# Optimization experiments

Measured on AMD Instinct MI355X. Metric: run time of the kernel, lower is better.

The kernel has to match this reference:

```python
import jax, jax.numpy as jnp
import numpy as np

EPS = 1e-5
GROUPS = 32


def setup_inputs() -> dict:
    key = jax.random.key(0)
    ks = jax.random.split(key, 12)
    b, c, h, w = 8, 256, 64, 64
    s = 1.0 / np.sqrt(c)
    return {
        "x": jax.random.normal(ks[0], (b, c, h, w), jnp.float32),
        "gn_w": jax.random.uniform(ks[1], (c,), jnp.float32, 0.5, 1.5),
        "gn_b": jax.random.normal(ks[2], (c,), jnp.float32) * 0.1,
        "wq": jax.random.normal(ks[3], (c, c), jnp.float32) * s,
        "bq": jax.random.normal(ks[4], (c,), jnp.float32) * 0.02,
        "wk": jax.random.normal(ks[5], (c, c), jnp.float32) * s,
        "bk": jax.random.normal(ks[6], (c,), jnp.float32) * 0.02,
        "wv": jax.random.normal(ks[7], (c, c), jnp.float32) * s,
        "bv": jax.random.normal(ks[8], (c,), jnp.float32) * 0.02,
        "wp": jax.random.normal(ks[9], (c, c), jnp.float32) * s,
        "bp": jax.random.normal(ks[10], (c,), jnp.float32) * 0.02,
        "gamma": jax.random.normal(ks[11], (1,), jnp.float32),
    }


def _group_norm(x, weight, bias):
    b, c, h, w = x.shape
    g = min(c, GROUPS)
    xg = x.reshape(b, g, c // g, h * w)
    mean = xg.mean(axis=(2, 3), keepdims=True)
    var = jnp.var(xg, axis=(2, 3), keepdims=True)
    xn = (xg - mean) * jax.lax.rsqrt(var + EPS)
    xn = xn.reshape(b, c, h, w)
    return xn * weight[None, :, None, None] + bias[None, :, None, None]


def reference(x, gn_w, gn_b, wq, bq, wk, bk, wv, bv, wp, bp, gamma):
    b, c, h, w = x.shape
    x_dash = _group_norm(x, gn_w, gn_b)           # (b,c,h,w)
    xf = x_dash.reshape(b, c, h * w)              # (b,c,n)
    # 1x1 convs == per-pixel linear maps over channels
    q = jnp.einsum('oc,bcn->bon', wq, xf) + bq[None, :, None]
    k = jnp.einsum('oc,bcn->bon', wk, xf) + bk[None, :, None]
    v = jnp.einsum('oc,bcn->bon', wv, xf) + bv[None, :, None]
    # attn[b,i,j] = <q[:,i], k[:,j]> / sqrt(c)
    attn = jnp.einsum('bci,bcj->bij', q, k) / jnp.sqrt(jnp.asarray(c, x.dtype))
    attn = jax.nn.softmax(attn, axis=-1)
    # out[b,c,i] = sum_j v[b,c,j] * attn[b,i,j]
    out = jnp.einsum('bcj,bij->bci', v, attn)
    out = jnp.einsum('oc,bcn->bon', wp, out) + bp[None, :, None]
    out = out.reshape(b, c, h, w)
    return x + gamma[0] * out
```

## Files before the change

kernel.cpp:

```cpp
#include <hip/hip_runtime.h>
#include <cstdint>
#include <cstddef>


#define NB   8
#define NC   256
#define NPIX 4096
#define CPG  8

typedef __attribute__((ext_vector_type(8))) short bf16x8;
typedef __attribute__((ext_vector_type(4))) short s16x4;
typedef __attribute__((ext_vector_type(8))) short s16x8;
typedef __attribute__((ext_vector_type(4))) float f32x4;

__device__ __forceinline__ short f2bf(float f) {
  union { float f; uint32_t u; } v; v.f = f;
  return (short)((v.u + 0x7fffu + ((v.u >> 16) & 1u)) >> 16);
}

__device__ __forceinline__ uint32_t cvtpk_bf(float a, float b) {
  uint32_t r;
  asm("v_cvt_pk_bf16_f32 %0, %1, %2" : "=v"(r) : "v"(a), "v"(b));
  return r;
}

__device__ __forceinline__ f32x4 mfma16(bf16x8 a, bf16x8 b, f32x4 c) {
  return __builtin_amdgcn_mfma_f32_16x16x32_bf16(a, b, c, 0, 0, 0);
}

__device__ __forceinline__ void gload_lds16(const short* g, short* l) {
  __builtin_amdgcn_global_load_lds(
      (const __attribute__((address_space(1))) void*)g,
      (__attribute__((address_space(3))) void*)l, 16, 0, 0);
}

__global__ __launch_bounds__(256) void wconv4(
    const float* __restrict__ w0, const float* __restrict__ w1,
    const float* __restrict__ w2, const float* __restrict__ w3,
    short* __restrict__ o0, short* __restrict__ o1,
    short* __restrict__ o2, short* __restrict__ o3) {
  int m = blockIdx.x >> 6;
  const float* w = (m == 0) ? w0 : (m == 1) ? w1 : (m == 2) ? w2 : w3;
  short* o = (m == 0) ? o0 : (m == 1) ? o1 : (m == 2) ? o2 : o3;
  int i = ((blockIdx.x & 63) * 256 + threadIdx.x) * 4;
  float4 v = *reinterpret_cast<const float4*>(w + i);
  s16x4 p;
  p[0] = f2bf(v.x); p[1] = f2bf(v.y); p[2] = f2bf(v.z); p[3] = f2bf(v.w);
  *reinterpret_cast<s16x4*>(o + i) = p;
}

__global__ __launch_bounds__(256) void gnorm(const float* __restrict__ x,
                                             const float* __restrict__ gw,
                                             const float* __restrict__ gb,
                                             short* __restrict__ xdt) {
  int b = blockIdx.x >> 5;
  int g = blockIdx.x & 31;
  const float* xp = x + ((size_t)b * NC + (size_t)g * CPG) * NPIX;
  int t = threadIdx.x;

  float s = 0.f, ss = 0.f;
  const float4* xp4 = reinterpret_cast<const float4*>(xp);
  for (int i = t; i < (CPG * NPIX) / 4; i += 256) {
    float4 v = xp4[i];
    s  += v.x + v.y + v.z + v.w;
    ss += v.x * v.x + v.y * v.y + v.z * v.z + v.w * v.w;
  }
  for (int m = 32; m; m >>= 1) { s += __shfl_xor(s, m); ss += __shfl_xor(ss, m); }
  __shared__ float red[10];
  int wid = t >> 6;
  if ((t & 63) == 0) { red[wid] = s; red[4 + wid] = ss; }
  __syncthreads();
  if (t == 0) {
    float a  = red[0] + red[1] + red[2] + red[3];
    float b2 = red[4] + red[5] + red[6] + red[7];
    float mean = a * (1.f / 32768.f);
    float var  = b2 * (1.f / 32768.f) - mean * mean;
    red[8] = mean;
    red[9] = rsqrtf(var + 1e-5f);
  }
  __syncthreads();
  float mean = red[8], rstd = red[9];

  float wv2[CPG], bv2[CPG];
  for (int cc = 0; cc < CPG; ++cc) {
    float wgt = gw[g * CPG + cc] * rstd;
    wv2[cc] = wgt;
    bv2[cc] = gb[g * CPG + cc] - mean * wgt;
  }
  for (int pix = t; pix < NPIX; pix += 256) {
    s16x8 pk;
    for (int cc = 0; cc < CPG; ++cc)
      pk[cc] = f2bf(fmaf(xp[cc * NPIX + pix], wv2[cc], bv2[cc]));
    *reinterpret_cast<s16x8*>(&xdt[((size_t)b * NPIX + pix) * NC + g * CPG]) = pk;
  }
}

__global__ __launch_bounds__(256) void qkv_gemm(
    const short* __restrict__ wq_bf, const short* __restrict__ wk_bf,
    const short* __restrict__ wv_bf,
    const float* __restrict__ bq, const float* __restrict__ bk,
    const float* __restrict__ bv,
    const short* __restrict__ xdt,
    short* __restrict__ qt, short* __restrict__ kt, short* __restrict__ vv) {
  int nt = blockIdx.x, b = blockIdx.y;

  __shared__ short xtile[64 * 256];
  __shared__ float bias_lds[3][256];
  int t = threadIdx.x;
  const short* xg = xdt + ((size_t)b * NPIX + nt * 64) * NC;
  for (int it = 0; it < 8; ++it) {
    int id = t + it * 256, row = id >> 5, part = id & 31;
    *reinterpret_cast<uint4*>(&xtile[row * 256 + (part ^ (row & 7)) * 8]) =
        *reinterpret_cast<const uint4*>(&xg[(size_t)row * 256 + part * 8]);
  }
  bias_lds[0][t] = bq[t];
  bias_lds[1][t] = bk[t];
  bias_lds[2][t] = bv[t];
  __syncthreads();

  int w = t >> 6, lane = t & 63, g = lane >> 4, lr = lane & 15;
  const short* Ws[3] = {wq_bf, wk_bf, wv_bf};

  for (int mi = 0; mi < 3; ++mi) {
    const short* W = Ws[mi];
    f32x4 acc[4][4];
    f32x4 zz = {0.f, 0.f, 0.f, 0.f};
    for (int i = 0; i < 4; ++i) for (int j = 0; j < 4; ++j) acc[i][j] = zz;

    for (int c0 = 0; c0 < 256; c0 += 32) {
      bf16x8 af[4], bfr[4];
      for (int mf = 0; mf < 4; ++mf)
        af[mf] = *reinterpret_cast<const bf16x8*>(
            &W[(size_t)(w * 64 + mf * 16 + lr) * 256 + c0 + g * 8]);
      for (int nf = 0; nf < 4; ++nf) {
        int row = nf * 16 + lr;
        bfr[nf] = *reinterpret_cast<const bf16x8*>(
            &xtile[row * 256 + (((c0 >> 3) + g) ^ (row & 7)) * 8]);
      }
      for (int mf = 0; mf < 4; ++mf)
        for (int nf = 0; nf < 4; ++nf)
          acc[mf][nf] = mfma16(af[mf], bfr[nf], acc[mf][nf]);
    }

    if (mi < 2) {
      short* outp = (mi == 0) ? qt : kt;
      for (int mf = 0; mf < 4; ++mf)
        for (int nf = 0; nf < 4; ++nf) {
          int ob = w * 64 + mf * 16 + g * 4;
          int n  = nt * 64 + nf * 16 + lr;
          s16x4 pk;
          for (int r = 0; r < 4; ++r)
            pk[r] = f2bf(acc[mf][nf][r] + bias_lds[mi][ob + r]);
          *reinterpret_cast<s16x4*>(&outp[((size_t)b * NPIX + n) * NC + ob]) = pk;
        }
    } else {
      for (int mf = 0; mf < 4; ++mf)
        for (int nf = 0; nf < 4; ++nf) {
          int ob = w * 64 + mf * 16 + g * 4;
          int n  = nt * 64 + nf * 16 + lr;
          for (int r = 0; r < 4; ++r)
            vv[((size_t)b * NC + ob + r) * NPIX + n] =
                f2bf(acc[mf][nf][r] + bias_lds[2][ob + r]);
        }
    }
  }
}

__global__ __launch_bounds__(256, 2) void attn(
    const short* __restrict__ qt, const short* __restrict__ kt,
    const short* __restrict__ vv, short* __restrict__ ot) {
  int b = blockIdx.x, itile = blockIdx.y;
  __shared__ short ktile[64 * 256];
  __shared__ short Pb[2][64 * 64];
  __shared__ float alpha_lds[2][64];
  __shared__ float exch[2][64];

  int t = threadIdx.x, w = t >> 6, lane = t & 63, g = lane >> 4, lr = lane & 15;
  int kk = w >> 1, qq = w & 1;
  int i0 = itile * 64;

  const short* ktg = kt + (size_t)b * NPIX * NC;

  for (int it = 0; it < 8; ++it) {
    int id = it * 256 + t, row = id >> 5, ch = id & 31;
    gload_lds16(ktg + row * 256 + (ch ^ (row & 7)) * 8, &ktile[id * 8]);
  }
  const short* kgp = ktg + 16384;

  bf16x8 qf[2][8];
  for (int qi = 0; qi < 2; ++qi) {
    const short* qrow =
        qt + ((size_t)b * NPIX + i0 + 32 * qq + 16 * qi + lr) * NC;
    for (int ks = 0; ks < 8; ++ks)
      qf[qi][ks] = *reinterpret_cast<const bf16x8*>(&qrow[ks * 32 + g * 8]);
  }

  const short* vp = vv + (size_t)b * NC * NPIX + (size_t)(w * 64 + lr) * NPIX + g * 8;

  int row0 = 32 * kk + lr, row1 = row0 + 16;
  int eidx[2], pwo[2][2];
  for (int qi = 0; qi < 2; ++qi) {
    int q_loc = 32 * qq + 16 * qi + lr;
    eidx[qi] = q_loc;
    for (int mt = 0; mt < 2; ++mt)
      pwo[qi][mt] = q_loc * 64 +
                    (((4 * kk + 2 * mt + (g >> 1)) ^ (q_loc & 7)) * 8) +
                    (g & 1) * 4;
  }
  int pr[4][2];
  for (int nf = 0; nf < 4; ++nf)
    for (int ks2 = 0; ks2 < 2; ++ks2) {
      int qc = nf * 16 + lr;
      pr[nf][ks2] = qc * 64 + (((ks2 * 4 + g) ^ (qc & 7)) * 8);
    }

  f32x4 zz = {0.f, 0.f, 0.f, 0.f};
  f32x4 oacc[4][4];
  for (int i = 0; i < 4; ++i) for (int j = 0; j < 4; ++j) oacc[i][j] = zz;
  bf16x8 va[2][4];
  float m_[2] = {-1e30f, -1e30f}, l_p[2] = {0.f, 0.f};

  const float sc = 0.0625f, L2E = 1.44269504f;
  const float SCL = sc * L2E;

  for (int jt = 0; jt < 64; ++jt) {
    int cur = jt & 1, prv = cur ^ 1;

    asm volatile("s_waitcnt vmcnt(0) lgkmcnt(0)" ::: "memory");
    __builtin_amdgcn_s_barrier();
    asm volatile("" ::: "memory");

    if (jt > 0) {
      float av[4];
      for (int nf = 0; nf < 4; ++nf) av[nf] = alpha_lds[prv][nf * 16 + lr];
      if (__any((av[0] != 1.f) | (av[1] != 1.f) | (av[2] != 1.f) | (av[3] != 1.f))) {
        for (int mf = 0; mf < 4; ++mf)
          for (int nf = 0; nf < 4; ++nf) oacc[mf][nf] *= av[nf];
      }
      __builtin_amdgcn_s_setprio(1);
      for (int ks2 = 0; ks2 < 2; ++ks2) {
        bf16x8 pb[4];
        for (int nf = 0; nf < 4; ++nf)
          pb[nf] = *reinterpret_cast<const bf16x8*>(&Pb[prv][pr[nf][ks2]]);
        for (int mf = 0; mf < 4; ++mf)
          for (int nf = 0; nf < 4; ++nf)
            oacc[mf][nf] = mfma16(va[ks2][mf], pb[nf], oacc[mf][nf]);
      }
      __builtin_amdgcn_s_setprio(0);
    }

    for (int ks2 = 0; ks2 < 2; ++ks2)
      for (int mf = 0; mf < 4; ++mf)
        va[ks2][mf] = *reinterpret_cast<const bf16x8*>(
            vp + (size_t)mf * (16 * NPIX) + ks2 * 32);
    vp += 64;

    f32x4 s[2][2];
    s[0][0] = zz; s[0][1] = zz; s[1][0] = zz; s[1][1] = zz;
    __builtin_amdgcn_s_setprio(1);
    for (int ks = 0; ks < 8; ++ks) {
      bf16x8 kf0 = *reinterpret_cast<const bf16x8*>(
          &ktile[row0 * 256 + (((ks * 4) + g) ^ (row0 & 7)) * 8]);
      bf16x8 kf1 = *reinterpret_cast<const bf16x8*>(
          &ktile[row1 * 256 + (((ks * 4) + g) ^ (row1 & 7)) * 8]);
      s[0][0] = mfma16(kf0, qf[0][ks], s[0][0]);
      s[0][1] = mfma16(kf0, qf[1][ks], s[0][1]);
      s[1][0] = mfma16(kf1, qf[0][ks], s[1][0]);
      s[1][1] = mfma16(kf1, qf[1][ks], s[1][1]);
    }
    __builtin_amdgcn_s_setprio(0);

    float mx[2];
    for (int qi = 0; qi < 2; ++qi) {
      float m0 = fmaxf(fmaxf(s[0][qi][0], s[0][qi][1]),
                       fmaxf(s[0][qi][2], s[0][qi][3]));
      float m1 = fmaxf(fmaxf(s[1][qi][0], s[1][qi][1]),
                       fmaxf(s[1][qi][2], s[1][qi][3]));
      float m = fmaxf(m0, m1);
      m = fmaxf(m, __shfl_xor(m, 16));
      m = fmaxf(m, __shfl_xor(m, 32));
      mx[qi] = m;
    }
    if (lane < 16) {
      exch[kk][32 * qq + lr]      = mx[0];
      exch[kk][32 * qq + 16 + lr] = mx[1];
    }

    asm volatile("s_waitcnt lgkmcnt(0)" ::: "memory");
    __builtin_amdgcn_s_barrier();
    asm volatile("" ::: "memory");

    for (int it = 0; it < 8; ++it) {
      int id = it * 256 + t, row = id >> 5, ch = id & 31;
      gload_lds16(kgp + row * 256 + (ch ^ (row & 7)) * 8, &ktile[id * 8]);
    }
    kgp += 16384;

    for (int qi = 0; qi < 2; ++qi) {
      float pm = fmaxf(mx[qi], exch[kk ^ 1][eidx[qi]]) * sc;
      float mn = (pm - m_[qi] <= 8.f) ? m_[qi] : pm;
      float alpha = exp2f((m_[qi] - mn) * L2E);
      float mnl = mn * L2E;
      float ps = 0.f;
      for (int mt = 0; mt < 2; ++mt) {
        float p0 = exp2f(fmaf(s[mt][qi][0], SCL, -mnl));
        float p1 = exp2f(fmaf(s[mt][qi][1], SCL, -mnl));
        float p2 = exp2f(fmaf(s[mt][qi][2], SCL, -mnl));
        float p3 = exp2f(fmaf(s[mt][qi][3], SCL, -mnl));
        ps += p0 + p1 + p2 + p3;
        uint2 pk;
        pk.x = cvtpk_bf(p0, p1);
        pk.y = cvtpk_bf(p2, p3);
        *reinterpret_cast<uint2*>(&Pb[cur][pwo[qi][mt]]) = pk;
      }
      l_p[qi] = l_p[qi] * alpha + ps;
      m_[qi] = mn;
      if (kk == 0 && lane < 16) alpha_lds[cur][eidx[qi]] = alpha;
    }
  }

  asm volatile("s_waitcnt vmcnt(0) lgkmcnt(0)" ::: "memory");
  __builtin_amdgcn_s_barrier();
  asm volatile("" ::: "memory");
  {
    float av[4];
    for (int nf = 0; nf < 4; ++nf) av[nf] = alpha_lds[1][nf * 16 + lr];
    if (__any((av[0] != 1.f) | (av[1] != 1.f) | (av[2] != 1.f) | (av[3] != 1.f))) {
      for (int mf = 0; mf < 4; ++mf)
        for (int nf = 0; nf < 4; ++nf) oacc[mf][nf] *= av[nf];
    }
    for (int ks2 = 0; ks2 < 2; ++ks2) {
      bf16x8 pb[4];
      for (int nf = 0; nf < 4; ++nf)
        pb[nf] = *reinterpret_cast<const bf16x8*>(&Pb[1][pr[nf][ks2]]);
      for (int mf = 0; mf < 4; ++mf)
        for (int nf = 0; nf < 4; ++nf)
          oacc[mf][nf] = mfma16(va[ks2][mf], pb[nf], oacc[mf][nf]);
    }
  }

  for (int qi = 0; qi < 2; ++qi) {
    float v = l_p[qi];
    v += __shfl_xor(v, 16);
    v += __shfl_xor(v, 32);
    l_p[qi] = v;
  }
  if (lane < 16) {
    exch[kk][32 * qq + lr]      = l_p[0];
    exch[kk][32 * qq + 16 + lr] = l_p[1];
  }
  __syncthreads();

  for (int nf = 0; nf < 4; ++nf) {
    int q = nf * 16 + lr;
    float inv = 1.f / (exch[0][q] + exch[1][q]);
    int i = i0 + q;
    for (int mf = 0; mf < 4; ++mf) {
      int cb = w * 64 + mf * 16 + g * 4;
      s16x4 pk;
      for (int r = 0; r < 4; ++r) pk[r] = f2bf(oacc[mf][nf][r] * inv);
      *reinterpret_cast<s16x4*>(&ot[((size_t)b * NPIX + i) * NC + cb]) = pk;
    }
  }
}

__global__ __launch_bounds__(256) void proj_res(
    const short* __restrict__ wp_bf, const float* __restrict__ bp,
    const short* __restrict__ ot, const float* __restrict__ x,
    const float* __restrict__ gamma, float* __restrict__ out) {
  int nt = blockIdx.x, b = blockIdx.y;
  __shared__ short otile[64 * 256];
  __shared__ float bias_lds[256];
  int t = threadIdx.x;
  const short* og = ot + ((size_t)b * NPIX + nt * 64) * NC;
  for (int itx = 0; itx < 8; ++itx) {
    int id = t + itx * 256, row = id >> 5, part = id & 31;
    *reinterpret_cast<uint4*>(&otile[row * 256 + (part ^ (row & 7)) * 8]) =
        *reinterpret_cast<const uint4*>(&og[(size_t)row * 256 + part * 8]);
  }
  bias_lds[t] = bp[t];
  __syncthreads();

  int w = t >> 6, lane = t & 63, g = lane >> 4, lr = lane & 15;
  f32x4 acc[4][4];
  f32x4 zz = {0.f, 0.f, 0.f, 0.f};
  for (int i = 0; i < 4; ++i) for (int j = 0; j < 4; ++j) acc[i][j] = zz;

  for (int c0 = 0; c0 < 256; c0 += 32) {
    bf16x8 af[4], bfr[4];
    for (int mf = 0; mf < 4; ++mf)
      af[mf] = *reinterpret_cast<const bf16x8*>(
          &wp_bf[(size_t)(w * 64 + mf * 16 + lr) * 256 + c0 + g * 8]);
    for (int nf = 0; nf < 4; ++nf) {
      int row = nf * 16 + lr;
      bfr[nf] = *reinterpret_cast<const bf16x8*>(
          &otile[row * 256 + (((c0 >> 3) + g) ^ (row & 7)) * 8]);
    }
    for (int mf = 0; mf < 4; ++mf)
      for (int nf = 0; nf < 4; ++nf)
        acc[mf][nf] = mfma16(af[mf], bfr[nf], acc[mf][nf]);
  }

  float gm = gamma[0];
  for (int mf = 0; mf < 4; ++mf)
    for (int nf = 0; nf < 4; ++nf) {
      int ob = w * 64 + mf * 16 + g * 4;
      int n  = nt * 64 + nf * 16 + lr;
      for (int r = 0; r < 4; ++r) {
        size_t idx = ((size_t)b * NC + ob + r) * NPIX + n;
        out[idx] = x[idx] + gm * (acc[mf][nf][r] + bias_lds[ob + r]);
      }
    }
}

extern "C" void kernel_launch(void* const* d_in, const int* in_sizes, int n_in,
                              void* d_out, int out_size, void* d_ws, size_t ws_size,
                              hipStream_t stream) {
  (void)in_sizes; (void)n_in; (void)out_size; (void)ws_size;
  const float* x     = (const float*)d_in[0];
  const float* gn_w  = (const float*)d_in[1];
  const float* gn_b  = (const float*)d_in[2];
  const float* wq    = (const float*)d_in[3];
  const float* bq    = (const float*)d_in[4];
  const float* wk    = (const float*)d_in[5];
  const float* bk    = (const float*)d_in[6];
  const float* wv    = (const float*)d_in[7];
  const float* bv    = (const float*)d_in[8];
  const float* wp    = (const float*)d_in[9];
  const float* bp    = (const float*)d_in[10];
  const float* gamma = (const float*)d_in[11];
  float* out = (float*)d_out;

  char* ws = (char*)d_ws;
  const size_t WSZ = 131072;
  const size_t TSZ = (size_t)NB * NPIX * NC * 2;
  short* wq_bf = (short*)(ws);
  short* wk_bf = (short*)(ws + WSZ);
  short* wv_bf = (short*)(ws + 2 * WSZ);
  short* wp_bf = (short*)(ws + 3 * WSZ);
  short* xdt   = (short*)(ws + 4 * WSZ);
  short* qt    = (short*)(ws + 4 * WSZ + TSZ);
  short* kt    = (short*)(ws + 4 * WSZ + 2 * TSZ);
  short* vv    = (short*)(ws + 4 * WSZ + 3 * TSZ);
  short* ot    = xdt;

  wconv4<<<256, 256, 0, stream>>>(wq, wk, wv, wp, wq_bf, wk_bf, wv_bf, wp_bf);

  gnorm<<<256, 256, 0, stream>>>(x, gn_w, gn_b, xdt);

  qkv_gemm<<<dim3(64, 8), 256, 0, stream>>>(wq_bf, wk_bf, wv_bf, bq, bk, bv,
                                            xdt, qt, kt, vv);

  attn<<<dim3(8, 64), 256, 0, stream>>>(qt, kt, vv, ot);

  proj_res<<<dim3(64, 8), 256, 0, stream>>>(wp_bf, bp, ot, x, gamma, out);
}
```

Baseline: 316.8 us.

## Decouple per-half-key softmax state in attention and widen groupnorm blocks

The attention kernel now keeps separate running max, sum and output accumulators for each pair of waves covering a key half. This removes the per-tile cross-wave max exchange through shared memory, and the max update and rescale run only when a score exceeds a lazy threshold. The PV MFMAs are split so each half's accumulation sits on a different side of the barrier, and the two partial results are merged with exp-weighted combination at the end. This doubles the output accumulator registers, which risks register pressure and spills at two blocks per CU. Separately, groupnorm runs with 1024-thread blocks instead of 256.

```diff
diff --git a/kernel.cpp b/kernel.cpp
--- a/kernel.cpp
+++ b/kernel.cpp
@@ -49,10 +49,10 @@
   *reinterpret_cast<s16x4*>(o + i) = p;
 }
 
-__global__ __launch_bounds__(256) void gnorm(const float* __restrict__ x,
-                                             const float* __restrict__ gw,
-                                             const float* __restrict__ gb,
-                                             short* __restrict__ xdt) {
+__global__ __launch_bounds__(1024) void gnorm(const float* __restrict__ x,
+                                              const float* __restrict__ gw,
+                                              const float* __restrict__ gb,
+                                              short* __restrict__ xdt) {
   int b = blockIdx.x >> 5;
   int g = blockIdx.x & 31;
   const float* xp = x + ((size_t)b * NC + (size_t)g * CPG) * NPIX;
@@ -60,26 +60,26 @@
 
   float s = 0.f, ss = 0.f;
   const float4* xp4 = reinterpret_cast<const float4*>(xp);
-  for (int i = t; i < (CPG * NPIX) / 4; i += 256) {
+  for (int i = t; i < (CPG * NPIX) / 4; i += 1024) {
     float4 v = xp4[i];
     s  += v.x + v.y + v.z + v.w;
     ss += v.x * v.x + v.y * v.y + v.z * v.z + v.w * v.w;
   }
   for (int m = 32; m; m >>= 1) { s += __shfl_xor(s, m); ss += __shfl_xor(ss, m); }
-  __shared__ float red[10];
+  __shared__ float red[34];
   int wid = t >> 6;
-  if ((t & 63) == 0) { red[wid] = s; red[4 + wid] = ss; }
+  if ((t & 63) == 0) { red[wid] = s; red[16 + wid] = ss; }
   __syncthreads();
   if (t == 0) {
-    float a  = red[0] + red[1] + red[2] + red[3];
-    float b2 = red[4] + red[5] + red[6] + red[7];
+    float a = 0.f, b2 = 0.f;
+    for (int i = 0; i < 16; ++i) { a += red[i]; b2 += red[16 + i]; }
     float mean = a * (1.f / 32768.f);
     float var  = b2 * (1.f / 32768.f) - mean * mean;
-    red[8] = mean;
-    red[9] = rsqrtf(var + 1e-5f);
+    red[32] = mean;
+    red[33] = rsqrtf(var + 1e-5f);
   }
   __syncthreads();
-  float mean = red[8], rstd = red[9];
+  float mean = red[32], rstd = red[33];
 
   float wv2[CPG], bv2[CPG];
   for (int cc = 0; cc < CPG; ++cc) {
@@ -87,7 +87,7 @@
     wv2[cc] = wgt;
     bv2[cc] = gb[g * CPG + cc] - mean * wgt;
   }
-  for (int pix = t; pix < NPIX; pix += 256) {
+  for (int pix = t; pix < NPIX; pix += 1024) {
     s16x8 pk;
     for (int cc = 0; cc < CPG; ++cc)
       pk[cc] = f2bf(fmaf(xp[cc * NPIX + pix], wv2[cc], bv2[cc]));
@@ -172,8 +172,9 @@
   int b = blockIdx.x, itile = blockIdx.y;
   __shared__ short ktile[64 * 256];
   __shared__ short Pb[2][64 * 64];
-  __shared__ float alpha_lds[2][64];
-  __shared__ float exch[2][64];
+  __shared__ float alpha_lds[2][2][64];
+  __shared__ float mfin[2][64];
+  __shared__ float lfin[2][64];
 
   int t = threadIdx.x, w = t >> 6, lane = t & 63, g = lane >> 4, lr = lane & 15;
   int kk = w >> 1, qq = w & 1;
@@ -195,17 +196,17 @@
       qf[qi][ks] = *reinterpret_cast<const bf16x8*>(&qrow[ks * 32 + g * 8]);
   }
 
-  const short* vp = vv + (size_t)b * NC * NPIX + (size_t)(w * 64 + lr) * NPIX + g * 8;
+  const short* vbase =
+      vv + (size_t)b * NC * NPIX + (size_t)(w * 64 + lr) * NPIX + g * 8;
 
   int row0 = 32 * kk + lr, row1 = row0 + 16;
-  int eidx[2], pwo[2][2];
-  for (int qi = 0; qi < 2; ++qi) {
-    int q_loc = 32 * qq + 16 * qi + lr;
-    eidx[qi] = q_loc;
-    for (int mt = 0; mt < 2; ++mt)
-      pwo[qi][mt] = q_loc * 64 +
-                    (((4 * kk + 2 * mt + (g >> 1)) ^ (q_loc & 7)) * 8) +
-                    (g & 1) * 4;
+  int pwo00, pwo01, pwo10, pwo11;
+  {
+    int q0 = 32 * qq + lr, q1 = q0 + 16;
+    pwo00 = q0 * 64 + (((4 * kk + 0 + (g >> 1)) ^ (q0 & 7)) * 8) + (g & 1) * 4;
+    pwo01 = q0 * 64 + (((4 * kk + 2 + (g >> 1)) ^ (q0 & 7)) * 8) + (g & 1) * 4;
+    pwo10 = q1 * 64 + (((4 * kk + 0 + (g >> 1)) ^ (q1 & 7)) * 8) + (g & 1) * 4;
+    pwo11 = q1 * 64 + (((4 * kk + 2 + (g >> 1)) ^ (q1 & 7)) * 8) + (g & 1) * 4;
   }
   int pr[4][2];
   for (int nf = 0; nf < 4; ++nf)
@@ -215,10 +216,13 @@
     }
 
   f32x4 zz = {0.f, 0.f, 0.f, 0.f};
-  f32x4 oacc[4][4];
-  for (int i = 0; i < 4; ++i) for (int j = 0; j < 4; ++j) oacc[i][j] = zz;
-  bf16x8 va[2][4];
-  float m_[2] = {-1e30f, -1e30f}, l_p[2] = {0.f, 0.f};
+  f32x4 oacc0[4][4], oacc1[4][4];
+  for (int i = 0; i < 4; ++i)
+    for (int j = 0; j < 4; ++j) { oacc0[i][j] = zz; oacc1[i][j] = zz; }
+  bf16x8 va0[4], va1[4];
+
+  float m0_ = 0.f, m1_ = 0.f, l0_ = 0.f, l1_ = 0.f;
+  float thr0 = 128.f, thr1 = 128.f;
 
   const float sc = 0.0625f, L2E = 1.44269504f;
   const float SCL = sc * L2E;
@@ -232,59 +236,45 @@
 
     if (jt > 0) {
       float av[4];
-      for (int nf = 0; nf < 4; ++nf) av[nf] = alpha_lds[prv][nf * 16 + lr];
+#pragma unroll
+      for (int nf = 0; nf < 4; ++nf) av[nf] = alpha_lds[prv][0][nf * 16 + lr];
       if (__any((av[0] != 1.f) | (av[1] != 1.f) | (av[2] != 1.f) | (av[3] != 1.f))) {
+#pragma unroll
         for (int mf = 0; mf < 4; ++mf)
-          for (int nf = 0; nf < 4; ++nf) oacc[mf][nf] *= av[nf];
+#pragma unroll
+          for (int nf = 0; nf < 4; ++nf) oacc0[mf][nf] *= av[nf];
       }
       __builtin_amdgcn_s_setprio(1);
-      for (int ks2 = 0; ks2 < 2; ++ks2) {
-        bf16x8 pb[4];
+      bf16x8 pb[4];
+#pragma unroll
+      for (int nf = 0; nf < 4; ++nf)
+        pb[nf] = *reinterpret_cast<const bf16x8*>(&Pb[prv][pr[nf][0]]);
+#pragma unroll
+      for (int mf = 0; mf < 4; ++mf)
+#pragma unroll
         for (int nf = 0; nf < 4; ++nf)
-          pb[nf] = *reinterpret_cast<const bf16x8*>(&Pb[prv][pr[nf][ks2]]);
-        for (int mf = 0; mf < 4; ++mf)
-          for (int nf = 0; nf < 4; ++nf)
-            oacc[mf][nf] = mfma16(va[ks2][mf], pb[nf], oacc[mf][nf]);
-      }
+          oacc0[mf][nf] = mfma16(va0[mf], pb[nf], oacc0[mf][nf]);
       __builtin_amdgcn_s_setprio(0);
-    }
-
-    for (int ks2 = 0; ks2 < 2; ++ks2)
-      for (int mf = 0; mf < 4; ++mf)
-        va[ks2][mf] = *reinterpret_cast<const bf16x8*>(
-            vp + (size_t)mf * (16 * NPIX) + ks2 * 32);
-    vp += 64;
-
-    f32x4 s[2][2];
-    s[0][0] = zz; s[0][1] = zz; s[1][0] = zz; s[1][1] = zz;
+      const short* vp = vbase + (size_t)(jt - 1) * 64 + 32;
+#pragma unroll
+      for (int mf = 0; mf < 4; ++mf)
+        va1[mf] = *reinterpret_cast<const bf16x8*>(vp + (size_t)mf * (16 * NPIX));
+    }
+
+    f32x4 s00 = zz, s01 = zz, s10 = zz, s11 = zz;
     __builtin_amdgcn_s_setprio(1);
+#pragma unroll
     for (int ks = 0; ks < 8; ++ks) {
       bf16x8 kf0 = *reinterpret_cast<const bf16x8*>(
           &ktile[row0 * 256 + (((ks * 4) + g) ^ (row0 & 7)) * 8]);
       bf16x8 kf1 = *reinterpret_cast<const bf16x8*>(
           &ktile[row1 * 256 + (((ks * 4) + g) ^ (row1 & 7)) * 8]);
-      s[0][0] = mfma16(kf0, qf[0][ks], s[0][0]);
-      s[0][1] = mfma16(kf0, qf[1][ks], s[0][1]);
-      s[1][0] = mfma16(kf1, qf[0][ks], s[1][0]);
-      s[1][1] = mfma16(kf1, qf[1][ks], s[1][1]);
+      s00 = mfma16(kf0, qf[0][ks], s00);
+      s01 = mfma16(kf0, qf[1][ks], s01);
+      s10 = mfma16(kf1, qf[0][ks], s10);
+      s11 = mfma16(kf1, qf[1][ks], s11);
     }
     __builtin_amdgcn_s_setprio(0);
-
-    float mx[2];
-    for (int qi = 0; qi < 2; ++qi) {
-      float m0 = fmaxf(fmaxf(s[0][qi][0], s[0][qi][1]),
-                       fmaxf(s[0][qi][2], s[0][qi][3]));
-      float m1 = fmaxf(fmaxf(s[1][qi][0], s[1][qi][1]),
-                       fmaxf(s[1][qi][2], s[1][qi][3]));
-      float m = fmaxf(m0, m1);
-      m = fmaxf(m, __shfl_xor(m, 16));
-      m = fmaxf(m, __shfl_xor(m, 32));
-      mx[qi] = m;
-    }
-    if (lane < 16) {
-      exch[kk][32 * qq + lr]      = mx[0];
-      exch[kk][32 * qq + 16 + lr] = mx[1];
-    }
 
     asm volatile("s_waitcnt lgkmcnt(0)" ::: "memory");
     __builtin_amdgcn_s_barrier();
@@ -296,69 +286,159 @@
     }
     kgp += 16384;
 
-    for (int qi = 0; qi < 2; ++qi) {
-      float pm = fmaxf(mx[qi], exch[kk ^ 1][eidx[qi]]) * sc;
-      float mn = (pm - m_[qi] <= 8.f) ? m_[qi] : pm;
-      float alpha = exp2f((m_[qi] - mn) * L2E);
-      float mnl = mn * L2E;
-      float ps = 0.f;
-      for (int mt = 0; mt < 2; ++mt) {
-        float p0 = exp2f(fmaf(s[mt][qi][0], SCL, -mnl));
-        float p1 = exp2f(fmaf(s[mt][qi][1], SCL, -mnl));
-        float p2 = exp2f(fmaf(s[mt][qi][2], SCL, -mnl));
-        float p3 = exp2f(fmaf(s[mt][qi][3], SCL, -mnl));
-        ps += p0 + p1 + p2 + p3;
-        uint2 pk;
-        pk.x = cvtpk_bf(p0, p1);
-        pk.y = cvtpk_bf(p2, p3);
-        *reinterpret_cast<uint2*>(&Pb[cur][pwo[qi][mt]]) = pk;
+    if (jt > 0) {
+      float av[4];
+#pragma unroll
+      for (int nf = 0; nf < 4; ++nf) av[nf] = alpha_lds[prv][1][nf * 16 + lr];
+      if (__any((av[0] != 1.f) | (av[1] != 1.f) | (av[2] != 1.f) | (av[3] != 1.f))) {
+#pragma unroll
+        for (int mf = 0; mf < 4; ++mf)
+#pragma unroll
+          for (int nf = 0; nf < 4; ++nf) oacc1[mf][nf] *= av[nf];
       }
-      l_p[qi] = l_p[qi] * alpha + ps;
-      m_[qi] = mn;
-      if (kk == 0 && lane < 16) alpha_lds[cur][eidx[qi]] = alpha;
-    }
-  }
-
+      __builtin_amdgcn_s_setprio(1);
+      bf16x8 pb[4];
+#pragma unroll
+      for (int nf = 0; nf < 4; ++nf)
+        pb[nf] = *reinterpret_cast<const bf16x8*>(&Pb[prv][pr[nf][1]]);
+#pragma unroll
+      for (int mf = 0; mf < 4; ++mf)
+#pragma unroll
+        for (int nf = 0; nf < 4; ++nf)
+          oacc1[mf][nf] = mfma16(va1[mf], pb[nf], oacc1[mf][nf]);
+      __builtin_amdgcn_s_setprio(0);
+    }
+
+    {
+      const short* vp = vbase + (size_t)jt * 64;
+#pragma unroll
+      for (int mf = 0; mf < 4; ++mf)
+        va0[mf] = *reinterpret_cast<const bf16x8*>(vp + (size_t)mf * (16 * NPIX));
+    }
+
+    float ym0 = fmaxf(fmaxf(fmaxf(s00[0], s00[1]), fmaxf(s00[2], s00[3])),
+                      fmaxf(fmaxf(s10[0], s10[1]), fmaxf(s10[2], s10[3])));
+    float ym1 = fmaxf(fmaxf(fmaxf(s01[0], s01[1]), fmaxf(s01[2], s01[3])),
+                      fmaxf(fmaxf(s11[0], s11[1]), fmaxf(s11[2], s11[3])));
+    float alpha0 = 1.f, alpha1 = 1.f;
+    if (__any((ym0 > thr0) | (ym1 > thr1))) {
+      float sm0 = fmaxf(ym0, __shfl_xor(ym0, 16));
+      sm0 = fmaxf(sm0, __shfl_xor(sm0, 32));
+      float sm1 = fmaxf(ym1, __shfl_xor(ym1, 16));
+      sm1 = fmaxf(sm1, __shfl_xor(sm1, 32));
+      float mn0 = fmaxf(m0_, sm0 * sc);
+      float mn1 = fmaxf(m1_, sm1 * sc);
+      alpha0 = exp2f((m0_ - mn0) * L2E);
+      alpha1 = exp2f((m1_ - mn1) * L2E);
+      m0_ = mn0; m1_ = mn1;
+      thr0 = (mn0 + 8.f) * 16.f;
+      thr1 = (mn1 + 8.f) * 16.f;
+    }
+    float ml0 = m0_ * L2E, ml1 = m1_ * L2E;
+    float ps0, ps1;
+    {
+      float p0 = exp2f(fmaf(s00[0], SCL, -ml0));
+      float p1 = exp2f(fmaf(s00[1], SCL, -ml0));
+      float p2 = exp2f(fmaf(s00[2], SCL, -ml0));
+      float p3 = exp2f(fmaf(s00[3], SCL, -ml0));
+      ps0 = (p0 + p1) + (p2 + p3);
+      uint2 pk; pk.x = cvtpk_bf(p0, p1); pk.y = cvtpk_bf(p2, p3);
+      *reinterpret_cast<uint2*>(&Pb[cur][pwo00]) = pk;
+      p0 = exp2f(fmaf(s10[0], SCL, -ml0));
+      p1 = exp2f(fmaf(s10[1], SCL, -ml0));
+      p2 = exp2f(fmaf(s10[2], SCL, -ml0));
+      p3 = exp2f(fmaf(s10[3], SCL, -ml0));
+      ps0 += (p0 + p1) + (p2 + p3);
+      pk.x = cvtpk_bf(p0, p1); pk.y = cvtpk_bf(p2, p3);
+      *reinterpret_cast<uint2*>(&Pb[cur][pwo01]) = pk;
+    }
+    {
+      float p0 = exp2f(fmaf(s01[0], SCL, -ml1));
+      float p1 = exp2f(fmaf(s01[1], SCL, -ml1));
+      float p2 = exp2f(fmaf(s01[2], SCL, -ml1));
+      float p3 = exp2f(fmaf(s01[3], SCL, -ml1));
+      ps1 = (p0 + p1) + (p2 + p3);
+      uint2 pk; pk.x = cvtpk_bf(p0, p1); pk.y = cvtpk_bf(p2, p3);
+      *reinterpret_cast<uint2*>(&Pb[cur][pwo10]) = pk;
+      p0 = exp2f(fmaf(s11[0], SCL, -ml1));
+      p1 = exp2f(fmaf(s11[1], SCL, -ml1));
+      p2 = exp2f(fmaf(s11[2], SCL, -ml1));
+      p3 = exp2f(fmaf(s11[3], SCL, -ml1));
+      ps1 += (p0 + p1) + (p2 + p3);
+      pk.x = cvtpk_bf(p0, p1); pk.y = cvtpk_bf(p2, p3);
+      *reinterpret_cast<uint2*>(&Pb[cur][pwo11]) = pk;
+    }
+    l0_ = l0_ * alpha0 + ps0;
+    l1_ = l1_ * alpha1 + ps1;
+    if (lane < 16) {
+      alpha_lds[cur][kk][32 * qq + lane]      = alpha0;
+      alpha_lds[cur][kk][32 * qq + 16 + lane] = alpha1;
+    }
+  }
+
+  {
+    const short* vp = vbase + (size_t)63 * 64 + 32;
+#pragma unroll
+    for (int mf = 0; mf < 4; ++mf)
+      va1[mf] = *reinterpret_cast<const bf16x8*>(vp + (size_t)mf * (16 * NPIX));
+  }
   asm volatile("s_waitcnt vmcnt(0) lgkmcnt(0)" ::: "memory");
   __builtin_amdgcn_s_barrier();
   asm volatile("" ::: "memory");
   {
     float av[4];
-    for (int nf = 0; nf < 4; ++nf) av[nf] = alpha_lds[1][nf * 16 + lr];
+#pragma unroll
+    for (int nf = 0; nf < 4; ++nf) av[nf] = alpha_lds[1][0][nf * 16 + lr];
     if (__any((av[0] != 1.f) | (av[1] != 1.f) | (av[2] != 1.f) | (av[3] != 1.f))) {
       for (int mf = 0; mf < 4; ++mf)
-        for (int nf = 0; nf < 4; ++nf) oacc[mf][nf] *= av[nf];
-    }
-    for (int ks2 = 0; ks2 < 2; ++ks2) {
-      bf16x8 pb[4];
+        for (int nf = 0; nf < 4; ++nf) oacc0[mf][nf] *= av[nf];
+    }
+    bf16x8 pb[4];
+#pragma unroll
+    for (int nf = 0; nf < 4; ++nf)
+      pb[nf] = *reinterpret_cast<const bf16x8*>(&Pb[1][pr[nf][0]]);
+    for (int mf = 0; mf < 4; ++mf)
       for (int nf = 0; nf < 4; ++nf)
-        pb[nf] = *reinterpret_cast<const bf16x8*>(&Pb[1][pr[nf][ks2]]);
-      for (int mf = 0; mf < 4; ++mf)
-        for (int nf = 0; nf < 4; ++nf)
-          oacc[mf][nf] = mfma16(va[ks2][mf], pb[nf], oacc[mf][nf]);
-    }
-  }
-
-  for (int qi = 0; qi < 2; ++qi) {
-    float v = l_p[qi];
-    v += __shfl_xor(v, 16);
-    v += __shfl_xor(v, 32);
-    l_p[qi] = v;
-  }
+        oacc0[mf][nf] = mfma16(va0[mf], pb[nf], oacc0[mf][nf]);
+#pragma unroll
+    for (int nf = 0; nf < 4; ++nf) av[nf] = alpha_lds[1][1][nf * 16 + lr];
+    if (__any((av[0] != 1.f) | (av[1] != 1.f) | (av[2] != 1.f) | (av[3] != 1.f))) {
+      for (int mf = 0; mf < 4; ++mf)
+        for (int nf = 0; nf < 4; ++nf) oacc1[mf][nf] *= av[nf];
+    }
+#pragma unroll
+    for (int nf = 0; nf < 4; ++nf)
+      pb[nf] = *reinterpret_cast<const bf16x8*>(&Pb[1][pr[nf][1]]);
+    for (int mf = 0; mf < 4; ++mf)
+      for (int nf = 0; nf < 4; ++nf)
+        oacc1[mf][nf] = mfma16(va1[mf], pb[nf], oacc1[mf][nf]);
+  }
+
+  l0_ += __shfl_xor(l0_, 16); l0_ += __shfl_xor(l0_, 32);
+  l1_ += __shfl_xor(l1_, 16); l1_ += __shfl_xor(l1_, 32);
   if (lane < 16) {
-    exch[kk][32 * qq + lr]      = l_p[0];
-    exch[kk][32 * qq + 16 + lr] = l_p[1];
+    mfin[kk][32 * qq + lane]      = m0_;
+    mfin[kk][32 * qq + 16 + lane] = m1_;
+    lfin[kk][32 * qq + lane]      = l0_;
+    lfin[kk][32 * qq + 16 + lane] = l1_;
   }
   __syncthreads();
 
   for (int nf = 0; nf < 4; ++nf) {
     int q = nf * 16 + lr;
-    float inv = 1.f / (exch[0][q] + exch[1][q]);
+    float m0 = mfin[0][q], m1 = mfin[1][q];
+    float l0 = lfin[0][q], l1 = lfin[1][q];
+    float M = fmaxf(m0, m1);
+    float f0 = exp2f((m0 - M) * L2E);
+    float f1 = exp2f((m1 - M) * L2E);
+    float inv = 1.f / (f0 * l0 + f1 * l1);
+    f0 *= inv; f1 *= inv;
     int i = i0 + q;
     for (int mf = 0; mf < 4; ++mf) {
       int cb = w * 64 + mf * 16 + g * 4;
       s16x4 pk;
-      for (int r = 0; r < 4; ++r) pk[r] = f2bf(oacc[mf][nf][r] * inv);
+      for (int r = 0; r < 4; ++r)
+        pk[r] = f2bf(f0 * oacc0[mf][nf][r] + f1 * oacc1[mf][nf][r]);
       *reinterpret_cast<s16x4*>(&ot[((size_t)b * NPIX + i) * NC + cb]) = pk;
     }
   }
@@ -446,7 +526,7 @@
 
   wconv4<<<256, 256, 0, stream>>>(wq, wk, wv, wp, wq_bf, wk_bf, wv_bf, wp_bf);
 
-  gnorm<<<256, 256, 0, stream>>>(x, gn_w, gn_b, xdt);
+  gnorm<<<256, 1024, 0, stream>>>(x, gn_w, gn_b, xdt);
 
   qkv_gemm<<<dim3(64, 8), 256, 0, stream>>>(wq_bf, wk_bf, wv_bf, bq, bk, bv,
                                             xdt, qt, kt, vv);
```

Result: slower. 1.007 ms (+218.0%).

## Split PV MFMA across attention loop halves and widen groupnorm blocks

Applied to the files above, without the earlier changes.

The attention loop now splits the P·V MFMA work into two halves. The first half runs before the QK^T scores, and the second runs after the K-tile prefetch is issued, behind a partial vmcnt wait. V fragment loads are staggered into va0/va1 so their global latency overlaps other work. The groupnorm kernel moves from 256 to 1024 threads per block with a wider reduction, to raise memory-level parallelism. Risks include extra register pressure, and a partial vmcnt count that depends on the exact number of outstanding loads.

```diff
diff --git a/kernel.cpp b/kernel.cpp
--- a/kernel.cpp
+++ b/kernel.cpp
@@ -49,10 +49,10 @@
   *reinterpret_cast<s16x4*>(o + i) = p;
 }
 
-__global__ __launch_bounds__(256) void gnorm(const float* __restrict__ x,
-                                             const float* __restrict__ gw,
-                                             const float* __restrict__ gb,
-                                             short* __restrict__ xdt) {
+__global__ __launch_bounds__(1024) void gnorm(const float* __restrict__ x,
+                                              const float* __restrict__ gw,
+                                              const float* __restrict__ gb,
+                                              short* __restrict__ xdt) {
   int b = blockIdx.x >> 5;
   int g = blockIdx.x & 31;
   const float* xp = x + ((size_t)b * NC + (size_t)g * CPG) * NPIX;
@@ -60,26 +60,26 @@
 
   float s = 0.f, ss = 0.f;
   const float4* xp4 = reinterpret_cast<const float4*>(xp);
-  for (int i = t; i < (CPG * NPIX) / 4; i += 256) {
+  for (int i = t; i < (CPG * NPIX) / 4; i += 1024) {
     float4 v = xp4[i];
     s  += v.x + v.y + v.z + v.w;
     ss += v.x * v.x + v.y * v.y + v.z * v.z + v.w * v.w;
   }
   for (int m = 32; m; m >>= 1) { s += __shfl_xor(s, m); ss += __shfl_xor(ss, m); }
-  __shared__ float red[10];
+  __shared__ float red[34];
   int wid = t >> 6;
-  if ((t & 63) == 0) { red[wid] = s; red[4 + wid] = ss; }
+  if ((t & 63) == 0) { red[wid] = s; red[16 + wid] = ss; }
   __syncthreads();
   if (t == 0) {
-    float a  = red[0] + red[1] + red[2] + red[3];
-    float b2 = red[4] + red[5] + red[6] + red[7];
+    float a = 0.f, b2 = 0.f;
+    for (int i = 0; i < 16; ++i) { a += red[i]; b2 += red[16 + i]; }
     float mean = a * (1.f / 32768.f);
     float var  = b2 * (1.f / 32768.f) - mean * mean;
-    red[8] = mean;
-    red[9] = rsqrtf(var + 1e-5f);
+    red[32] = mean;
+    red[33] = rsqrtf(var + 1e-5f);
   }
   __syncthreads();
-  float mean = red[8], rstd = red[9];
+  float mean = red[32], rstd = red[33];
 
   float wv2[CPG], bv2[CPG];
   for (int cc = 0; cc < CPG; ++cc) {
@@ -87,7 +87,7 @@
     wv2[cc] = wgt;
     bv2[cc] = gb[g * CPG + cc] - mean * wgt;
   }
-  for (int pix = t; pix < NPIX; pix += 256) {
+  for (int pix = t; pix < NPIX; pix += 1024) {
     s16x8 pk;
     for (int cc = 0; cc < CPG; ++cc)
       pk[cc] = f2bf(fmaf(xp[cc * NPIX + pix], wv2[cc], bv2[cc]));
@@ -195,7 +195,8 @@
       qf[qi][ks] = *reinterpret_cast<const bf16x8*>(&qrow[ks * 32 + g * 8]);
   }
 
-  const short* vp = vv + (size_t)b * NC * NPIX + (size_t)(w * 64 + lr) * NPIX + g * 8;
+  const short* vbase =
+      vv + (size_t)b * NC * NPIX + (size_t)(w * 64 + lr) * NPIX + g * 8;
 
   int row0 = 32 * kk + lr, row1 = row0 + 16;
   int eidx[2], pwo[2][2];
@@ -217,7 +218,7 @@
   f32x4 zz = {0.f, 0.f, 0.f, 0.f};
   f32x4 oacc[4][4];
   for (int i = 0; i < 4; ++i) for (int j = 0; j < 4; ++j) oacc[i][j] = zz;
-  bf16x8 va[2][4];
+  bf16x8 va0[4], va1[4];
   float m_[2] = {-1e30f, -1e30f}, l_p[2] = {0.f, 0.f};
 
   const float sc = 0.0625f, L2E = 1.44269504f;
@@ -232,32 +233,35 @@
 
     if (jt > 0) {
       float av[4];
+#pragma unroll
       for (int nf = 0; nf < 4; ++nf) av[nf] = alpha_lds[prv][nf * 16 + lr];
       if (__any((av[0] != 1.f) | (av[1] != 1.f) | (av[2] != 1.f) | (av[3] != 1.f))) {
+#pragma unroll
         for (int mf = 0; mf < 4; ++mf)
+#pragma unroll
           for (int nf = 0; nf < 4; ++nf) oacc[mf][nf] *= av[nf];
       }
       __builtin_amdgcn_s_setprio(1);
-      for (int ks2 = 0; ks2 < 2; ++ks2) {
-        bf16x8 pb[4];
+      bf16x8 pb[4];
+#pragma unroll
+      for (int nf = 0; nf < 4; ++nf)
+        pb[nf] = *reinterpret_cast<const bf16x8*>(&Pb[prv][pr[nf][0]]);
+#pragma unroll
+      for (int mf = 0; mf < 4; ++mf)
+#pragma unroll
         for (int nf = 0; nf < 4; ++nf)
-          pb[nf] = *reinterpret_cast<const bf16x8*>(&Pb[prv][pr[nf][ks2]]);
-        for (int mf = 0; mf < 4; ++mf)
-          for (int nf = 0; nf < 4; ++nf)
-            oacc[mf][nf] = mfma16(va[ks2][mf], pb[nf], oacc[mf][nf]);
-      }
+          oacc[mf][nf] = mfma16(va0[mf], pb[nf], oacc[mf][nf]);
       __builtin_amdgcn_s_setprio(0);
-    }
-
-    for (int ks2 = 0; ks2 < 2; ++ks2)
-      for (int mf = 0; mf < 4; ++mf)
-        va[ks2][mf] = *reinterpret_cast<const bf16x8*>(
-            vp + (size_t)mf * (16 * NPIX) + ks2 * 32);
-    vp += 64;
+      const short* vp = vbase + (size_t)(jt - 1) * 64 + 32;
+#pragma unroll
+      for (int mf = 0; mf < 4; ++mf)
+        va1[mf] = *reinterpret_cast<const bf16x8*>(vp + (size_t)mf * (16 * NPIX));
+    }
 
     f32x4 s[2][2];
     s[0][0] = zz; s[0][1] = zz; s[1][0] = zz; s[1][1] = zz;
     __builtin_amdgcn_s_setprio(1);
+#pragma unroll
     for (int ks = 0; ks < 8; ++ks) {
       bf16x8 kf0 = *reinterpret_cast<const bf16x8*>(
           &ktile[row0 * 256 + (((ks * 4) + g) ^ (row0 & 7)) * 8]);
@@ -271,6 +275,7 @@
     __builtin_amdgcn_s_setprio(0);
 
     float mx[2];
+#pragma unroll
     for (int qi = 0; qi < 2; ++qi) {
       float m0 = fmaxf(fmaxf(s[0][qi][0], s[0][qi][1]),
                        fmaxf(s[0][qi][2], s[0][qi][3]));
@@ -296,18 +301,42 @@
     }
     kgp += 16384;
 
+    if (jt > 0) {
+      asm volatile("s_waitcnt vmcnt(8)" ::: "memory");
+      __builtin_amdgcn_s_setprio(1);
+      bf16x8 pb[4];
+#pragma unroll
+      for (int nf = 0; nf < 4; ++nf)
+        pb[nf] = *reinterpret_cast<const bf16x8*>(&Pb[prv][pr[nf][1]]);
+#pragma unroll
+      for (int mf = 0; mf < 4; ++mf)
+#pragma unroll
+        for (int nf = 0; nf < 4; ++nf)
+          oacc[mf][nf] = mfma16(va1[mf], pb[nf], oacc[mf][nf]);
+      __builtin_amdgcn_s_setprio(0);
+    }
+
+    {
+      const short* vp = vbase + (size_t)jt * 64;
+#pragma unroll
+      for (int mf = 0; mf < 4; ++mf)
+        va0[mf] = *reinterpret_cast<const bf16x8*>(vp + (size_t)mf * (16 * NPIX));
+    }
+
+#pragma unroll
     for (int qi = 0; qi < 2; ++qi) {
       float pm = fmaxf(mx[qi], exch[kk ^ 1][eidx[qi]]) * sc;
       float mn = (pm - m_[qi] <= 8.f) ? m_[qi] : pm;
       float alpha = exp2f((m_[qi] - mn) * L2E);
       float mnl = mn * L2E;
       float ps = 0.f;
+#pragma unroll
       for (int mt = 0; mt < 2; ++mt) {
         float p0 = exp2f(fmaf(s[mt][qi][0], SCL, -mnl));
         float p1 = exp2f(fmaf(s[mt][qi][1], SCL, -mnl));
         float p2 = exp2f(fmaf(s[mt][qi][2], SCL, -mnl));
         float p3 = exp2f(fmaf(s[mt][qi][3], SCL, -mnl));
-        ps += p0 + p1 + p2 + p3;
+        ps += (p0 + p1) + (p2 + p3);
         uint2 pk;
         pk.x = cvtpk_bf(p0, p1);
         pk.y = cvtpk_bf(p2, p3);
@@ -319,26 +348,39 @@
     }
   }
 
+  {
+    const short* vp = vbase + (size_t)63 * 64 + 32;
+#pragma unroll
+    for (int mf = 0; mf < 4; ++mf)
+      va1[mf] = *reinterpret_cast<const bf16x8*>(vp + (size_t)mf * (16 * NPIX));
+  }
   asm volatile("s_waitcnt vmcnt(0) lgkmcnt(0)" ::: "memory");
   __builtin_amdgcn_s_barrier();
   asm volatile("" ::: "memory");
   {
     float av[4];
+#pragma unroll
     for (int nf = 0; nf < 4; ++nf) av[nf] = alpha_lds[1][nf * 16 + lr];
     if (__any((av[0] != 1.f) | (av[1] != 1.f) | (av[2] != 1.f) | (av[3] != 1.f))) {
       for (int mf = 0; mf < 4; ++mf)
         for (int nf = 0; nf < 4; ++nf) oacc[mf][nf] *= av[nf];
     }
-    for (int ks2 = 0; ks2 < 2; ++ks2) {
-      bf16x8 pb[4];
+    bf16x8 pb[4];
+#pragma unroll
+    for (int nf = 0; nf < 4; ++nf)
+      pb[nf] = *reinterpret_cast<const bf16x8*>(&Pb[1][pr[nf][0]]);
+    for (int mf = 0; mf < 4; ++mf)
       for (int nf = 0; nf < 4; ++nf)
-        pb[nf] = *reinterpret_cast<const bf16x8*>(&Pb[1][pr[nf][ks2]]);
-      for (int mf = 0; mf < 4; ++mf)
-        for (int nf = 0; nf < 4; ++nf)
-          oacc[mf][nf] = mfma16(va[ks2][mf], pb[nf], oacc[mf][nf]);
-    }
-  }
-
+        oacc[mf][nf] = mfma16(va0[mf], pb[nf], oacc[mf][nf]);
+#pragma unroll
+    for (int nf = 0; nf < 4; ++nf)
+      pb[nf] = *reinterpret_cast<const bf16x8*>(&Pb[1][pr[nf][1]]);
+    for (int mf = 0; mf < 4; ++mf)
+      for (int nf = 0; nf < 4; ++nf)
+        oacc[mf][nf] = mfma16(va1[mf], pb[nf], oacc[mf][nf]);
+  }
+
+#pragma unroll
   for (int qi = 0; qi < 2; ++qi) {
     float v = l_p[qi];
     v += __shfl_xor(v, 16);
@@ -446,7 +488,7 @@
 
   wconv4<<<256, 256, 0, stream>>>(wq, wk, wv, wp, wq_bf, wk_bf, wv_bf, wp_bf);
 
-  gnorm<<<256, 256, 0, stream>>>(x, gn_w, gn_b, xdt);
+  gnorm<<<256, 1024, 0, stream>>>(x, gn_w, gn_b, xdt);
 
   qkv_gemm<<<dim3(64, 8), 256, 0, stream>>>(wq_bf, wk_bf, wv_bf, bq, bk, bv,
                                             xdt, qt, kt, vv);
```

Measured after the change: 284.2 us. -10.3%, faster.
